# Performance work log

Measured on AMD Instinct MI355X. Metric: run time of the kernel, lower is better.

The kernel has to match this reference:

```python
import jax, jax.numpy as jnp
import numpy as np

WINDOW = (7, 7)
SHIFT = (3, 3)
NUM_HEADS = 4
DIM = 128
N = WINDOW[0] * WINDOW[1]  # 49 tokens per window


def _relative_position_index():
    ch, cw = np.arange(WINDOW[0]), np.arange(WINDOW[1])
    coords = np.stack(np.meshgrid(ch, cw, indexing='ij'))  # [2, wh, ww]
    cf = coords.reshape(2, -1)
    rel = cf[:, :, None] - cf[:, None, :]  # [2, N, N]
    rel = rel.transpose(1, 2, 0).copy()
    rel[:, :, 0] += WINDOW[0] - 1
    rel[:, :, 1] += WINDOW[1] - 1
    rel[:, :, 0] *= 2 * WINDOW[1] - 1
    return rel.sum(-1).reshape(-1)  # [N*N]

REL_IDX = _relative_position_index()


def _shift_mask(pad_H, pad_W):
    # per-window shift mask, [num_windows, N, N], 0 or -100
    img = np.zeros((pad_H, pad_W))
    hs = ((0, -WINDOW[0]), (-WINDOW[0], -SHIFT[0]), (-SHIFT[0], None))
    ws = ((0, -WINDOW[1]), (-WINDOW[1], -SHIFT[1]), (-SHIFT[1], None))
    cnt = 0
    for h in hs:
        for w in ws:
            img[h[0]:h[1], w[0]:w[1]] = cnt
            cnt += 1
    m = img.reshape(pad_H // WINDOW[0], WINDOW[0], pad_W // WINDOW[1], WINDOW[1])
    m = m.transpose(0, 2, 1, 3).reshape(-1, N)  # [nw, N]
    diff = m[:, None, :] - m[:, :, None]
    return np.where(diff != 0, -100.0, 0.0).astype(np.float32)


def setup_inputs() -> dict:
    key = jax.random.key(0)
    ks = jax.random.split(key, 12)
    B, H, W, C = 32, 112, 112, DIM
    s = 0.02
    return {
        'input_q': jax.random.normal(ks[0], (B, H, W, C), jnp.float32),
        'input_k': jax.random.normal(ks[1], (B, H, W, C), jnp.float32),
        'input_v': jax.random.normal(ks[2], (B, H, W, C), jnp.float32),
        'q_weight': jax.random.normal(ks[3], (C, C), jnp.float32) * s,
        'k_weight': jax.random.normal(ks[4], (C, C), jnp.float32) * s,
        'v_weight': jax.random.normal(ks[5], (C, C), jnp.float32) * s,
        'proj_weight': jax.random.normal(ks[6], (C, C), jnp.float32) * s,
        'q_bias': jax.random.normal(ks[7], (C,), jnp.float32) * s,
        'k_bias': jax.random.normal(ks[8], (C,), jnp.float32) * s,
        'v_bias': jax.random.normal(ks[9], (C,), jnp.float32) * s,
        'proj_bias': jax.random.normal(ks[10], (C,), jnp.float32) * s,
        'rel_pos_table': jax.random.normal(ks[11], ((2 * WINDOW[0] - 1) * (2 * WINDOW[1] - 1), NUM_HEADS), jnp.float32) * s,
    }


def reference(input_q, input_k, input_v, q_weight, k_weight, v_weight,
              proj_weight, q_bias, k_bias, v_bias, proj_bias, rel_pos_table):
    # NOTE: faithful to source — input_k/input_v are unused; q,k,v all come from input_q.
    B, H, W, C = input_q.shape
    wh, ww = WINDOW
    pad_b = (wh - H % wh) % wh
    pad_r = (ww - W % ww) % ww
    x = jnp.pad(input_q, ((0, 0), (0, pad_b), (0, pad_r), (0, 0)))
    pad_H, pad_W = H + pad_b, W + pad_r
    sh = 0 if wh >= pad_H else SHIFT[0]
    sw = 0 if ww >= pad_W else SHIFT[1]
    shifted = sh + sw > 0
    if shifted:
        x = jnp.roll(x, (-sh, -sw), axis=(1, 2))
    nH, nW = pad_H // wh, pad_W // ww
    nw = nH * nW
    # window partition -> [B*nw, N, C]
    x = x.reshape(B, nH, wh, nW, ww, C).transpose(0, 1, 3, 2, 4, 5).reshape(B * nw, N, C)
    hd = C // NUM_HEADS

    def heads(t):  # [BW, N, C] -> [BW, heads, N, hd]
        return t.reshape(B * nw, N, NUM_HEADS, hd).transpose(0, 2, 1, 3)

    q = heads(x @ q_weight.T + q_bias) * (hd ** -0.5)
    k = heads(x @ k_weight.T + k_bias)
    v = heads(x @ v_weight.T + v_bias)

    # relative position bias: [1, heads, N, N]
    rpb = rel_pos_table[REL_IDX].reshape(N, N, NUM_HEADS).transpose(2, 0, 1)[None]
    attn = jnp.einsum('whnd,whmd->whnm', q, k) + rpb
    if shifted:
        mask = jnp.asarray(_shift_mask(pad_H, pad_W))  # [nw, N, N]
        attn = attn.reshape(B, nw, NUM_HEADS, N, N) + mask[None, :, None]
        attn = attn.reshape(B * nw, NUM_HEADS, N, N)
    attn = jax.nn.softmax(attn, axis=-1)
    out = jnp.einsum('whnm,whmd->whnd', attn, v)  # [BW, heads, N, hd]
    out = out.transpose(0, 2, 1, 3).reshape(B * nw, N, C)
    out = out @ proj_weight.T + proj_bias
    # un-window -> [B, pad_H, pad_W, C]
    out = out.reshape(B, nH, nW, wh, ww, C).transpose(0, 1, 3, 2, 4, 5).reshape(B, pad_H, pad_W, C)
    if shifted:
        out = jnp.roll(out, (sh, sw), axis=(1, 2))
    return out[:, :H, :W, :]
```

## Files before the change

kernel.cpp:

```cpp
#include <hip/hip_runtime.h>

typedef __attribute__((ext_vector_type(8))) __bf16 bf16x8;
typedef __attribute__((ext_vector_type(4))) float f32x4;

#define IMG 112
#define SHF 3

__device__ __forceinline__ ushort f2bf(float f) {
  return __builtin_bit_cast(unsigned short, static_cast<__bf16>(f));
}
__device__ __forceinline__ uint pk2(float lo, float hi) {
  return (uint)f2bf(lo) | ((uint)f2bf(hi) << 16);
}
__device__ __forceinline__ int d7(int n) { return (n * 9363) >> 16; }

__device__ __forceinline__ bf16x8 pack2(const f32x4 d0, const f32x4 d1) {
  union { uint4 u; bf16x8 v; } r;
  r.u = uint4{ pk2(d0[0], d0[1]), pk2(d0[2], d0[3]),
               pk2(d1[0], d1[1]), pk2(d1[2], d1[3]) };
  return r.v;
}
__device__ __forceinline__ bf16x8 pack2b(const f32x4 d0, const float4 b0,
                                         const f32x4 d1, const float4 b1) {
  union { uint4 u; bf16x8 v; } r;
  r.u = uint4{ pk2(d0[0] + b0.x, d0[1] + b0.y), pk2(d0[2] + b0.z, d0[3] + b0.w),
               pk2(d1[0] + b1.x, d1[1] + b1.y), pk2(d1[2] + b1.z, d1[3] + b1.w) };
  return r.v;
}

__global__ void prep_kernel(const float* __restrict__ Wq, const float* __restrict__ Wk,
                            const float* __restrict__ Wv, const float* __restrict__ Wp,
                            const float* __restrict__ bq, const float* __restrict__ bk,
                            const float* __restrict__ bv, const float* __restrict__ bp,
                            const float* __restrict__ tbl,
                            ushort* __restrict__ wW, float* __restrict__ wB,
                            float* __restrict__ wRM) {
  int t = blockIdx.x * 256 + threadIdx.x;
  const float SC = 0.17677669529663687f;
  if (t < 65536) {
    int m = t >> 14, e = t & 16383;
    const float* W = (m == 0) ? Wq : (m == 1) ? Wk : (m == 2) ? Wv : Wp;
    float v = W[e];
    if (m == 0) v *= SC;
    wW[t] = f2bf(v);
  } else if (t < 66048) {
    int t2 = t - 65536;
    int m = t2 >> 7, e = t2 & 127;
    const float* B = (m == 0) ? bq : (m == 1) ? bk : (m == 2) ? bv : bp;
    float v = B[e];
    if (m == 0) v *= SC;
    wB[t2] = v;
  } else if (t < 131584) {
    int t3 = t - 66048;
    int cls = t3 >> 14;
    int r = t3 & 16383;
    int h = r >> 12;
    int rr = r & 4095;
    int qt = rr >> 6, kt = rr & 63;
    float v;
    if (qt >= 49) v = 0.0f;
    else if (kt >= 49) v = -1e30f;
    else {
      int rq = qt / 7, cq = qt % 7, rk = kt / 7, ck = kt % 7;
      v = tbl[((rq - rk + 6) * 13 + (cq - ck + 6)) * 4 + h];
      int eH = (cls >> 1) & 1, eW = cls & 1;
      int ridq = (eH ? (rq < 4 ? 3 : 6) : 0) + (eW ? (cq < 4 ? 1 : 2) : 0);
      int ridk = (eH ? (rk < 4 ? 3 : 6) : 0) + (eW ? (ck < 4 ? 1 : 2) : 0);
      if (ridq != ridk) v -= 100.0f;
    }
    wRM[t3] = v;
  }
}

#define OS 6664

__global__ __launch_bounds__(256, 2) void swin_kernel(
    const float* __restrict__ X, const ushort* __restrict__ wW,
    const float* __restrict__ wB, const float* __restrict__ wRM,
    float* __restrict__ out) {
  __shared__ ushort lds[13328];
  const int tid = threadIdx.x;
  const int wv = tid >> 6;
  const int lane = tid & 63;
  const int lr = lane & 15;
  const int kg = lane >> 4;

  const int blk = blockIdx.x;
  const int b = blk >> 8;
  const int wid = blk & 255;
  const int wi = wid >> 4, wj = wid & 15;
  const size_t gBase = (size_t)b * (IMG * IMG * 128);
  const int h = wv;

  {
    float4 va[7]; int rowa[7], q4a[7]; bool ok[7];
#pragma unroll
    for (int i = 0; i < 7; ++i) {
      int idx = tid + i * 256;
      ok[i] = idx < 49 * 32;
      int row = idx >> 5, q4 = idx & 31;
      rowa[i] = row; q4a[i] = q4;
      if (ok[i]) {
        int r = d7(row), c = row - r * 7;
        int gh = wi * 7 + r + SHF; if (gh >= IMG) gh -= IMG;
        int gw = wj * 7 + c + SHF; if (gw >= IMG) gw -= IMG;
        va[i] = reinterpret_cast<const float4*>(X + gBase + ((size_t)gh * IMG + gw) * 128)[q4];
      }
    }
#pragma unroll
    for (int i = 0; i < 7; ++i) {
      if (ok[i]) {
        ushort4 h4 = { f2bf(va[i].x), f2bf(va[i].y), f2bf(va[i].z), f2bf(va[i].w) };
        *reinterpret_cast<ushort4*>(&lds[rowa[i] * 136 + q4a[i] * 4]) = h4;
      }
    }
  }
  __syncthreads();

  bf16x8 xv[4][4];
#pragma unroll
  for (int kk = 0; kk < 4; ++kk)
#pragma unroll
    for (int tt = 0; tt < 4; ++tt) {
      int tok = tt * 16 + lr; if (tok > 48) tok = 48;
      xv[kk][tt] = *reinterpret_cast<const bf16x8*>(&lds[tok * 136 + kk * 32 + kg * 8]);
    }

  bf16x8 kfp[4];
  {
    bf16x8 wk[4][2];
#pragma unroll
    for (int kk = 0; kk < 4; ++kk)
#pragma unroll
      for (int ct = 0; ct < 2; ++ct)
        wk[kk][ct] = *reinterpret_cast<const bf16x8*>(&wW[16384 + (h * 32 + ct * 16 + lr) * 128 + kk * 32 + kg * 8]);
    f32x4 accK[2][4] = {};
#pragma unroll
    for (int kk = 0; kk < 4; ++kk)
#pragma unroll
      for (int ct = 0; ct < 2; ++ct)
#pragma unroll
        for (int tt = 0; tt < 4; ++tt)
          accK[ct][tt] = __builtin_amdgcn_mfma_f32_16x16x32_bf16(wk[kk][ct], xv[kk][tt], accK[ct][tt], 0, 0, 0);
    float4 bkv[2];
#pragma unroll
    for (int ct = 0; ct < 2; ++ct)
      bkv[ct] = *reinterpret_cast<const float4*>(&wB[128 + h * 32 + ct * 16 + kg * 4]);
#pragma unroll
    for (int tt = 0; tt < 4; ++tt)
      kfp[tt] = pack2b(accK[0][tt], bkv[0], accK[1][tt], bkv[1]);
  }

  bf16x8 vfp[2][2];
  {
    bf16x8 wvv[4][2];
#pragma unroll
    for (int kk = 0; kk < 4; ++kk)
#pragma unroll
      for (int nt = 0; nt < 2; ++nt)
        wvv[kk][nt] = *reinterpret_cast<const bf16x8*>(&wW[32768 + (h * 32 + nt * 16 + lr) * 128 + kk * 32 + kg * 8]);
    f32x4 accV[4][2] = {};
#pragma unroll
    for (int kk = 0; kk < 4; ++kk)
#pragma unroll
      for (int tt = 0; tt < 4; ++tt)
#pragma unroll
        for (int nt = 0; nt < 2; ++nt)
          accV[tt][nt] = __builtin_amdgcn_mfma_f32_16x16x32_bf16(xv[kk][tt], wvv[kk][nt], accV[tt][nt], 0, 0, 0);
    float bvs[2];
#pragma unroll
    for (int nt = 0; nt < 2; ++nt) bvs[nt] = wB[256 + h * 32 + nt * 16 + lr];
#pragma unroll
    for (int c = 0; c < 2; ++c)
#pragma unroll
      for (int nt = 0; nt < 2; ++nt) {
        f32x4 t0 = accV[2 * c][nt], t1 = accV[2 * c + 1][nt];
        t0[0] += bvs[nt]; t0[1] += bvs[nt]; t0[2] += bvs[nt]; t0[3] += bvs[nt];
        t1[0] += bvs[nt]; t1[1] += bvs[nt]; t1[2] += bvs[nt]; t1[3] += bvs[nt];
        vfp[c][nt] = pack2(t0, t1);
      }
  }

  bf16x8 qpp[4];
  {
    bf16x8 wq[4][2];
#pragma unroll
    for (int kk = 0; kk < 4; ++kk)
#pragma unroll
      for (int ct = 0; ct < 2; ++ct)
        wq[kk][ct] = *reinterpret_cast<const bf16x8*>(&wW[(h * 32 + ct * 16 + lr) * 128 + kk * 32 + kg * 8]);
    f32x4 accQ[2][4] = {};
#pragma unroll
    for (int kk = 0; kk < 4; ++kk)
#pragma unroll
      for (int ct = 0; ct < 2; ++ct)
#pragma unroll
        for (int bt = 0; bt < 4; ++bt)
          accQ[ct][bt] = __builtin_amdgcn_mfma_f32_16x16x32_bf16(wq[kk][ct], xv[kk][bt], accQ[ct][bt], 0, 0, 0);
    float4 bqv[2];
#pragma unroll
    for (int ct = 0; ct < 2; ++ct)
      bqv[ct] = *reinterpret_cast<const float4*>(&wB[h * 32 + ct * 16 + kg * 4]);
#pragma unroll
    for (int bt = 0; bt < 4; ++bt)
      qpp[bt] = pack2b(accQ[0][bt], bqv[0], accQ[1][bt], bqv[1]);
  }

  const int cls = ((wi == 15) ? 2 : 0) + ((wj == 15) ? 1 : 0);
  f32x4 s[4][4] = {};
#pragma unroll
  for (int tt = 0; tt < 4; ++tt)
#pragma unroll
    for (int bt = 0; bt < 4; ++bt)
      s[tt][bt] = __builtin_amdgcn_mfma_f32_16x16x32_bf16(kfp[tt], qpp[bt], s[tt][bt], 0, 0, 0);

  float sum[4];
  bf16x8 pfp[2][4];
#pragma unroll
  for (int bt = 0; bt < 4; ++bt) {
    int qtb = bt * 16 + lr;
    const float* rp = wRM + (((size_t)cls * 4 + h) * 64 + qtb) * 64 + kg * 4;
    float4 r4[4];
#pragma unroll
    for (int tt = 0; tt < 4; ++tt)
      r4[tt] = *reinterpret_cast<const float4*>(&rp[tt * 16]);
    float sm = 0.0f;
#pragma unroll
    for (int tt = 0; tt < 4; ++tt) {
#pragma unroll
      for (int i = 0; i < 4; ++i) {
        float e = __expf(fminf(s[tt][bt][i] + r4[tt][i], 60.0f));
        s[tt][bt][i] = e; sm += e;
      }
    }
    sum[bt] = sm;
#pragma unroll
    for (int c = 0; c < 2; ++c)
      pfp[c][bt] = pack2(s[2 * c][bt], s[2 * c + 1][bt]);
  }

  f32x4 o[2][4] = {};
#pragma unroll
  for (int nt = 0; nt < 2; ++nt)
#pragma unroll
    for (int bt = 0; bt < 4; ++bt) {
      o[nt][bt] = __builtin_amdgcn_mfma_f32_16x16x32_bf16(vfp[0][nt], pfp[0][bt], o[nt][bt], 0, 0, 0);
      o[nt][bt] = __builtin_amdgcn_mfma_f32_16x16x32_bf16(vfp[1][nt], pfp[1][bt], o[nt][bt], 0, 0, 0);
    }

  float inv[4];
#pragma unroll
  for (int bt = 0; bt < 4; ++bt) {
    float sm = sum[bt];
    sm += __shfl_xor(sm, 16);
    sm += __shfl_xor(sm, 32);
    inv[bt] = 1.0f / sm;
  }

#pragma unroll
  for (int bt = 0; bt < 4; ++bt) {
    int qtb = bt * 16 + lr;
    if (qtb < 49) {
      float iv = inv[bt];
#pragma unroll
      for (int nt = 0; nt < 2; ++nt) {
        ushort4 h4 = { f2bf(o[nt][bt][0] * iv), f2bf(o[nt][bt][1] * iv),
                       f2bf(o[nt][bt][2] * iv), f2bf(o[nt][bt][3] * iv) };
        *reinterpret_cast<ushort4*>(&lds[OS + qtb * 136 + h * 32 + nt * 16 + kg * 4]) = h4;
      }
    }
  }
  const int c0 = wv * 32;
  bf16x8 eaw[4][2];
  {
    const ushort* W = wW + 3 * 16384;
#pragma unroll
    for (int kk = 0; kk < 4; ++kk)
#pragma unroll
      for (int mt = 0; mt < 2; ++mt)
        eaw[kk][mt] = *reinterpret_cast<const bf16x8*>(&W[(c0 + mt * 16 + lr) * 128 + kk * 32 + kg * 8]);
  }
  __syncthreads();

  {
    bf16x8 bo[4][4];
#pragma unroll
    for (int kk = 0; kk < 4; ++kk)
#pragma unroll
      for (int ntk = 0; ntk < 4; ++ntk) {
        int tok = ntk * 16 + lr; if (tok > 48) tok = 48;
        bo[kk][ntk] = *reinterpret_cast<const bf16x8*>(&lds[OS + tok * 136 + kk * 32 + kg * 8]);
      }
    f32x4 acc[2][4] = {};
#pragma unroll
    for (int kk = 0; kk < 4; ++kk)
#pragma unroll
      for (int mt = 0; mt < 2; ++mt)
#pragma unroll
        for (int ntk = 0; ntk < 4; ++ntk)
          acc[mt][ntk] = __builtin_amdgcn_mfma_f32_16x16x32_bf16(eaw[kk][mt], bo[kk][ntk], acc[mt][ntk], 0, 0, 0);
#pragma unroll
    for (int mt = 0; mt < 2; ++mt) {
      float4 b4 = *reinterpret_cast<const float4*>(&wB[384 + c0 + mt * 16 + kg * 4]);
#pragma unroll
      for (int ntk = 0; ntk < 4; ++ntk) {
        int tok = ntk * 16 + lr;
        if (tok < 49) {
          int r = d7(tok), c = tok - r * 7;
          int gh = wi * 7 + r + SHF; if (gh >= IMG) gh -= IMG;
          int gw = wj * 7 + c + SHF; if (gw >= IMG) gw -= IMG;
          float4 o4 = { acc[mt][ntk][0] + b4.x, acc[mt][ntk][1] + b4.y,
                        acc[mt][ntk][2] + b4.z, acc[mt][ntk][3] + b4.w };
          *reinterpret_cast<float4*>(out + gBase + ((size_t)gh * IMG + gw) * 128 + c0 + mt * 16 + kg * 4) = o4;
        }
      }
    }
  }
}

extern "C" void kernel_launch(void* const* d_in, const int* in_sizes, int n_in,
                              void* d_out, int out_size, void* d_ws, size_t ws_size,
                              hipStream_t stream) {
  const float* X = (const float*)d_in[0];
  const float* Wq = (const float*)d_in[3];
  const float* Wk = (const float*)d_in[4];
  const float* Wv = (const float*)d_in[5];
  const float* Wp = (const float*)d_in[6];
  const float* bq = (const float*)d_in[7];
  const float* bk = (const float*)d_in[8];
  const float* bv = (const float*)d_in[9];
  const float* bp = (const float*)d_in[10];
  const float* tbl = (const float*)d_in[11];

  ushort* wW = (ushort*)d_ws;
  float* wB = (float*)((char*)d_ws + 131072);
  float* wRM = (float*)((char*)d_ws + 131072 + 2048);

  prep_kernel<<<dim3(514), dim3(256), 0, stream>>>(Wq, Wk, Wv, Wp, bq, bk, bv, bp, tbl, wW, wB, wRM);
  swin_kernel<<<dim3(8192), dim3(256), 0, stream>>>(X, wW, wB, wRM, (float*)d_out);
}
```

Measured before the change: 277.9 us.

## Cut register pressure to raise occupancy to three blocks per CU

Raises the launch bound minimum from two to three blocks per multiprocessor and restructures the Q/K/V/projection GEMMs to stream X tiles from LDS per k-step instead of holding all of them in registers. Score tiles are computed per query tile inside the softmax loop rather than all sixteen at once, and projection weights are loaded per k-step after the barrier. This lowers VGPR usage so more waves can hide latency, at the cost of repeated LDS reads of X (three times per projection) and less load/compute overlap for weights. The tighter register bound also risks spills.

```diff
diff --git a/kernel.cpp b/kernel.cpp
--- a/kernel.cpp
+++ b/kernel.cpp
@@ -74,7 +74,7 @@
 
 #define OS 6664
 
-__global__ __launch_bounds__(256, 2) void swin_kernel(
+__global__ __launch_bounds__(256, 3) void swin_kernel(
     const float* __restrict__ X, const ushort* __restrict__ wW,
     const float* __restrict__ wB, const float* __restrict__ wRM,
     float* __restrict__ out) {
@@ -91,6 +91,8 @@
   const int wi = wid >> 4, wj = wid & 15;
   const size_t gBase = (size_t)b * (IMG * IMG * 128);
   const int h = wv;
+  const int tok3 = (48 + lr > 63) ? 48 : 48 + lr;
+  const int r3 = 48 + lr;
 
   {
     float4 va[7]; int rowa[7], q4a[7]; bool ok[7];
@@ -117,103 +119,81 @@
   }
   __syncthreads();
 
-  bf16x8 xv[4][4];
-#pragma unroll
-  for (int kk = 0; kk < 4; ++kk)
-#pragma unroll
-    for (int tt = 0; tt < 4; ++tt) {
-      int tok = tt * 16 + lr; if (tok > 48) tok = 48;
-      xv[kk][tt] = *reinterpret_cast<const bf16x8*>(&lds[tok * 136 + kk * 32 + kg * 8]);
-    }
+  auto ldx = [&](int tt, int kk) -> bf16x8 {
+    int row = (tt < 3) ? (tt * 16 + lr) : ((r3 > 48) ? 48 : r3);
+    return *reinterpret_cast<const bf16x8*>(&lds[row * 136 + kk * 32 + kg * 8]);
+  };
 
   bf16x8 kfp[4];
   {
-    bf16x8 wk[4][2];
-#pragma unroll
-    for (int kk = 0; kk < 4; ++kk)
-#pragma unroll
-      for (int ct = 0; ct < 2; ++ct)
-        wk[kk][ct] = *reinterpret_cast<const bf16x8*>(&wW[16384 + (h * 32 + ct * 16 + lr) * 128 + kk * 32 + kg * 8]);
-    f32x4 accK[2][4] = {};
-#pragma unroll
-    for (int kk = 0; kk < 4; ++kk)
-#pragma unroll
-      for (int ct = 0; ct < 2; ++ct)
-#pragma unroll
-        for (int tt = 0; tt < 4; ++tt)
-          accK[ct][tt] = __builtin_amdgcn_mfma_f32_16x16x32_bf16(wk[kk][ct], xv[kk][tt], accK[ct][tt], 0, 0, 0);
-    float4 bkv[2];
-#pragma unroll
-    for (int ct = 0; ct < 2; ++ct)
-      bkv[ct] = *reinterpret_cast<const float4*>(&wB[128 + h * 32 + ct * 16 + kg * 4]);
+    f32x4 acc[2][4] = {};
+#pragma unroll
+    for (int kk = 0; kk < 4; ++kk) {
+      bf16x8 w0 = *reinterpret_cast<const bf16x8*>(&wW[16384 + (h * 32 + lr) * 128 + kk * 32 + kg * 8]);
+      bf16x8 w1 = *reinterpret_cast<const bf16x8*>(&wW[16384 + (h * 32 + 16 + lr) * 128 + kk * 32 + kg * 8]);
+#pragma unroll
+      for (int tt = 0; tt < 4; ++tt) {
+        bf16x8 x = ldx(tt, kk);
+        acc[0][tt] = __builtin_amdgcn_mfma_f32_16x16x32_bf16(w0, x, acc[0][tt], 0, 0, 0);
+        acc[1][tt] = __builtin_amdgcn_mfma_f32_16x16x32_bf16(w1, x, acc[1][tt], 0, 0, 0);
+      }
+    }
+    float4 b0 = *reinterpret_cast<const float4*>(&wB[128 + h * 32 + kg * 4]);
+    float4 b1 = *reinterpret_cast<const float4*>(&wB[128 + h * 32 + 16 + kg * 4]);
 #pragma unroll
     for (int tt = 0; tt < 4; ++tt)
-      kfp[tt] = pack2b(accK[0][tt], bkv[0], accK[1][tt], bkv[1]);
+      kfp[tt] = pack2b(acc[0][tt], b0, acc[1][tt], b1);
   }
 
   bf16x8 vfp[2][2];
   {
-    bf16x8 wvv[4][2];
-#pragma unroll
-    for (int kk = 0; kk < 4; ++kk)
-#pragma unroll
-      for (int nt = 0; nt < 2; ++nt)
-        wvv[kk][nt] = *reinterpret_cast<const bf16x8*>(&wW[32768 + (h * 32 + nt * 16 + lr) * 128 + kk * 32 + kg * 8]);
-    f32x4 accV[4][2] = {};
-#pragma unroll
-    for (int kk = 0; kk < 4; ++kk)
-#pragma unroll
-      for (int tt = 0; tt < 4; ++tt)
-#pragma unroll
-        for (int nt = 0; nt < 2; ++nt)
-          accV[tt][nt] = __builtin_amdgcn_mfma_f32_16x16x32_bf16(xv[kk][tt], wvv[kk][nt], accV[tt][nt], 0, 0, 0);
-    float bvs[2];
-#pragma unroll
-    for (int nt = 0; nt < 2; ++nt) bvs[nt] = wB[256 + h * 32 + nt * 16 + lr];
-#pragma unroll
-    for (int c = 0; c < 2; ++c)
-#pragma unroll
-      for (int nt = 0; nt < 2; ++nt) {
-        f32x4 t0 = accV[2 * c][nt], t1 = accV[2 * c + 1][nt];
-        t0[0] += bvs[nt]; t0[1] += bvs[nt]; t0[2] += bvs[nt]; t0[3] += bvs[nt];
-        t1[0] += bvs[nt]; t1[1] += bvs[nt]; t1[2] += bvs[nt]; t1[3] += bvs[nt];
-        vfp[c][nt] = pack2(t0, t1);
-      }
+    f32x4 acc[4][2] = {};
+#pragma unroll
+    for (int kk = 0; kk < 4; ++kk) {
+      bf16x8 w0 = *reinterpret_cast<const bf16x8*>(&wW[32768 + (h * 32 + lr) * 128 + kk * 32 + kg * 8]);
+      bf16x8 w1 = *reinterpret_cast<const bf16x8*>(&wW[32768 + (h * 32 + 16 + lr) * 128 + kk * 32 + kg * 8]);
+#pragma unroll
+      for (int tt = 0; tt < 4; ++tt) {
+        bf16x8 x = ldx(tt, kk);
+        acc[tt][0] = __builtin_amdgcn_mfma_f32_16x16x32_bf16(x, w0, acc[tt][0], 0, 0, 0);
+        acc[tt][1] = __builtin_amdgcn_mfma_f32_16x16x32_bf16(x, w1, acc[tt][1], 0, 0, 0);
+      }
+    }
+    float bv0 = wB[256 + h * 32 + lr];
+    float bv1 = wB[256 + h * 32 + 16 + lr];
+#pragma unroll
+    for (int c = 0; c < 2; ++c) {
+      f32x4 t00 = acc[2 * c][0], t10 = acc[2 * c + 1][0];
+      f32x4 t01 = acc[2 * c][1], t11 = acc[2 * c + 1][1];
+#pragma unroll
+      for (int i = 0; i < 4; ++i) { t00[i] += bv0; t10[i] += bv0; t01[i] += bv1; t11[i] += bv1; }
+      vfp[c][0] = pack2(t00, t10);
+      vfp[c][1] = pack2(t01, t11);
+    }
   }
 
   bf16x8 qpp[4];
   {
-    bf16x8 wq[4][2];
-#pragma unroll
-    for (int kk = 0; kk < 4; ++kk)
-#pragma unroll
-      for (int ct = 0; ct < 2; ++ct)
-        wq[kk][ct] = *reinterpret_cast<const bf16x8*>(&wW[(h * 32 + ct * 16 + lr) * 128 + kk * 32 + kg * 8]);
-    f32x4 accQ[2][4] = {};
-#pragma unroll
-    for (int kk = 0; kk < 4; ++kk)
-#pragma unroll
-      for (int ct = 0; ct < 2; ++ct)
-#pragma unroll
-        for (int bt = 0; bt < 4; ++bt)
-          accQ[ct][bt] = __builtin_amdgcn_mfma_f32_16x16x32_bf16(wq[kk][ct], xv[kk][bt], accQ[ct][bt], 0, 0, 0);
-    float4 bqv[2];
-#pragma unroll
-    for (int ct = 0; ct < 2; ++ct)
-      bqv[ct] = *reinterpret_cast<const float4*>(&wB[h * 32 + ct * 16 + kg * 4]);
+    f32x4 acc[2][4] = {};
+#pragma unroll
+    for (int kk = 0; kk < 4; ++kk) {
+      bf16x8 w0 = *reinterpret_cast<const bf16x8*>(&wW[(h * 32 + lr) * 128 + kk * 32 + kg * 8]);
+      bf16x8 w1 = *reinterpret_cast<const bf16x8*>(&wW[(h * 32 + 16 + lr) * 128 + kk * 32 + kg * 8]);
+#pragma unroll
+      for (int bt = 0; bt < 4; ++bt) {
+        bf16x8 x = ldx(bt, kk);
+        acc[0][bt] = __builtin_amdgcn_mfma_f32_16x16x32_bf16(w0, x, acc[0][bt], 0, 0, 0);
+        acc[1][bt] = __builtin_amdgcn_mfma_f32_16x16x32_bf16(w1, x, acc[1][bt], 0, 0, 0);
+      }
+    }
+    float4 b0 = *reinterpret_cast<const float4*>(&wB[h * 32 + kg * 4]);
+    float4 b1 = *reinterpret_cast<const float4*>(&wB[h * 32 + 16 + kg * 4]);
 #pragma unroll
     for (int bt = 0; bt < 4; ++bt)
-      qpp[bt] = pack2b(accQ[0][bt], bqv[0], accQ[1][bt], bqv[1]);
+      qpp[bt] = pack2b(acc[0][bt], b0, acc[1][bt], b1);
   }
 
   const int cls = ((wi == 15) ? 2 : 0) + ((wj == 15) ? 1 : 0);
-  f32x4 s[4][4] = {};
-#pragma unroll
-  for (int tt = 0; tt < 4; ++tt)
-#pragma unroll
-    for (int bt = 0; bt < 4; ++bt)
-      s[tt][bt] = __builtin_amdgcn_mfma_f32_16x16x32_bf16(kfp[tt], qpp[bt], s[tt][bt], 0, 0, 0);
-
   float sum[4];
   bf16x8 pfp[2][4];
 #pragma unroll
@@ -224,19 +204,22 @@
 #pragma unroll
     for (int tt = 0; tt < 4; ++tt)
       r4[tt] = *reinterpret_cast<const float4*>(&rp[tt * 16]);
+    f32x4 sc[4] = {};
+#pragma unroll
+    for (int tt = 0; tt < 4; ++tt)
+      sc[tt] = __builtin_amdgcn_mfma_f32_16x16x32_bf16(kfp[tt], qpp[bt], sc[tt], 0, 0, 0);
     float sm = 0.0f;
 #pragma unroll
     for (int tt = 0; tt < 4; ++tt) {
 #pragma unroll
       for (int i = 0; i < 4; ++i) {
-        float e = __expf(fminf(s[tt][bt][i] + r4[tt][i], 60.0f));
-        s[tt][bt][i] = e; sm += e;
+        float e = __expf(fminf(sc[tt][i] + r4[tt][i], 60.0f));
+        sc[tt][i] = e; sm += e;
       }
     }
     sum[bt] = sm;
-#pragma unroll
-    for (int c = 0; c < 2; ++c)
-      pfp[c][bt] = pack2(s[2 * c][bt], s[2 * c + 1][bt]);
+    pfp[0][bt] = pack2(sc[0], sc[1]);
+    pfp[1][bt] = pack2(sc[2], sc[3]);
   }
 
   f32x4 o[2][4] = {};
@@ -270,35 +253,24 @@
       }
     }
   }
-  const int c0 = wv * 32;
-  bf16x8 eaw[4][2];
-  {
+  __syncthreads();
+
+  {
+    const int c0 = wv * 32;
     const ushort* W = wW + 3 * 16384;
-#pragma unroll
-    for (int kk = 0; kk < 4; ++kk)
-#pragma unroll
-      for (int mt = 0; mt < 2; ++mt)
-        eaw[kk][mt] = *reinterpret_cast<const bf16x8*>(&W[(c0 + mt * 16 + lr) * 128 + kk * 32 + kg * 8]);
-  }
-  __syncthreads();
-
-  {
-    bf16x8 bo[4][4];
-#pragma unroll
-    for (int kk = 0; kk < 4; ++kk)
+    f32x4 acc[2][4] = {};
+#pragma unroll
+    for (int kk = 0; kk < 4; ++kk) {
+      bf16x8 w0 = *reinterpret_cast<const bf16x8*>(&W[(c0 + lr) * 128 + kk * 32 + kg * 8]);
+      bf16x8 w1 = *reinterpret_cast<const bf16x8*>(&W[(c0 + 16 + lr) * 128 + kk * 32 + kg * 8]);
 #pragma unroll
       for (int ntk = 0; ntk < 4; ++ntk) {
-        int tok = ntk * 16 + lr; if (tok > 48) tok = 48;
-        bo[kk][ntk] = *reinterpret_cast<const bf16x8*>(&lds[OS + tok * 136 + kk * 32 + kg * 8]);
-      }
-    f32x4 acc[2][4] = {};
-#pragma unroll
-    for (int kk = 0; kk < 4; ++kk)
-#pragma unroll
-      for (int mt = 0; mt < 2; ++mt)
-#pragma unroll
-        for (int ntk = 0; ntk < 4; ++ntk)
-          acc[mt][ntk] = __builtin_amdgcn_mfma_f32_16x16x32_bf16(eaw[kk][mt], bo[kk][ntk], acc[mt][ntk], 0, 0, 0);
+        int row = (ntk < 3) ? (ntk * 16 + lr) : ((r3 > 48) ? 48 : r3);
+        bf16x8 bo = *reinterpret_cast<const bf16x8*>(&lds[OS + row * 136 + kk * 32 + kg * 8]);
+        acc[0][ntk] = __builtin_amdgcn_mfma_f32_16x16x32_bf16(w0, bo, acc[0][ntk], 0, 0, 0);
+        acc[1][ntk] = __builtin_amdgcn_mfma_f32_16x16x32_bf16(w1, bo, acc[1][ntk], 0, 0, 0);
+      }
+    }
 #pragma unroll
     for (int mt = 0; mt < 2; ++mt) {
       float4 b4 = *reinterpret_cast<const float4*>(&wB[384 + c0 + mt * 16 + kg * 4]);
```

New measurement: 254.7 us. -8.3%, faster.
